# Optimization experiments

Measured on AMD Instinct MI355X. Metric: run time of the kernel, lower is better.

Reference implementation:

```python
import jax, jax.numpy as jnp
import numpy as np

B, S, D_MODEL, H, DK, DV, DOUT = 8, 2048, 1024, 1, 512, 512, 1024
EPS = 1e-6
TEMP = DK ** 0.5


def _ln(x, g, b):
    # LayerNorm over last dim, eps=1e-6, affine
    m = jnp.mean(x, axis=-1, keepdims=True)
    v = jnp.mean((x - m) ** 2, axis=-1, keepdims=True)
    return (x - m) * jax.lax.rsqrt(v + EPS) * g + b


def setup_inputs() -> dict:
    key = jax.random.key(0)
    ks = jax.random.split(key, 16)
    s = 0.02
    return {
        "q": jax.random.normal(ks[0], (B, S, D_MODEL), jnp.float32),
        "k": jax.random.normal(ks[1], (B, S, D_MODEL), jnp.float32),
        "v": jax.random.normal(ks[2], (B, S, D_MODEL), jnp.float32),
        "mask": jnp.ones((B, S, S), jnp.int32),
        "Wq": jax.random.normal(ks[3], (D_MODEL, H * DK), jnp.float32) * s,
        "bq": jnp.zeros((H * DK,), jnp.float32),
        "Wk": jax.random.normal(ks[4], (D_MODEL, H * DK), jnp.float32) * s,
        "bk": jnp.zeros((H * DK,), jnp.float32),
        "Wv": jax.random.normal(ks[5], (D_MODEL, H * DV), jnp.float32) * s,
        "bv": jnp.zeros((H * DV,), jnp.float32),
        "g_q": jnp.ones((H * DK,), jnp.float32),
        "be_q": jnp.zeros((H * DK,), jnp.float32),
        "g_k": jnp.ones((H * DK,), jnp.float32),
        "be_k": jnp.zeros((H * DK,), jnp.float32),
        "g_v": jnp.ones((H * DV,), jnp.float32),
        "be_v": jnp.zeros((H * DV,), jnp.float32),
        "W1": jax.random.normal(ks[6], (H * DV, H * DV), jnp.float32) * s,
        "b1": jnp.zeros((H * DV,), jnp.float32),
        "W2": jax.random.normal(ks[7], (H * DV, DOUT), jnp.float32) * s,
        "b2": jnp.zeros((DOUT,), jnp.float32),
    }


def reference(q, k, v, mask, Wq, bq, Wk, bk, Wv, bv, g_q, be_q, g_k, be_k, g_v, be_v, W1, b1, W2, b2):
    # QKV projections, viewed as (B, S, H, d)
    qp = (q @ Wq + bq).reshape(B, S, H, DK)
    kp = (k @ Wk + bk).reshape(B, S, H, DK)
    vp = (v @ Wv + bv).reshape(B, S, H, DV)
    residual = qp
    # per-(token,head) LayerNorm over last dim (valid only because H == 1 in source)
    qn = jnp.swapaxes(_ln(qp, g_q, be_q), 1, 2)  # (B, H, S, DK)
    kn = jnp.swapaxes(_ln(kp, g_k, be_k), 1, 2)
    vn = jnp.swapaxes(_ln(vp, g_v, be_v), 1, 2)
    # scaled dot-product attention with mask
    scores = jnp.einsum('bhqd,bhkd->bhqk', qn / TEMP, kn)
    scores = jnp.where(mask[:, None, :, :] == 0, -1e9, scores)
    attn = jax.nn.softmax(scores, axis=-1)
    out = jnp.einsum('bhqk,bhkd->bhqd', attn, vn)
    out = jnp.swapaxes(out, 1, 2).reshape(B, S, H * DV)
    # trailing 2-layer MLP
    out = jax.nn.relu(out @ W1 + b1) @ W2 + b2
    return (out, residual, jnp.squeeze(attn))
```

## Files before the change

### kernel.cpp

```cpp
#include <hip/hip_runtime.h>
#include <hip/hip_bf16.h>

typedef __attribute__((ext_vector_type(8))) short short8;
typedef __attribute__((ext_vector_type(4))) short short4v;
typedef __attribute__((ext_vector_type(4))) float f32x4;

#define INV_TEMP 0.044194173824159216f

__device__ __forceinline__ ushort f2bf(float f) {
  unsigned u = __float_as_uint(f);
  unsigned r = (u + 0x7FFFu + ((u >> 16) & 1u)) >> 16;
  return (ushort)r;
}
__device__ __forceinline__ float bf2f(ushort u) {
  union { unsigned i; float f; } x; x.i = ((unsigned)u) << 16; return x.f;
}

__device__ __forceinline__ void gload_lds16(const void* g, void* l) {
  __builtin_amdgcn_global_load_lds(
      (const __attribute__((address_space(1))) unsigned int*)(unsigned long long)(uintptr_t)g,
      (__attribute__((address_space(3))) unsigned int*)(unsigned)(uintptr_t)l,
      16, 0, 0);
}

__global__ __launch_bounds__(256)
void transpose_cvt_w(const float* __restrict__ W, ushort* __restrict__ WT, int K, int N) {
  __shared__ float tile[32][33];
  const int n0 = blockIdx.x * 32, k0 = blockIdx.y * 32;
  const int tx = threadIdx.x & 31, ty = threadIdx.x >> 5;
  #pragma unroll
  for (int i = ty; i < 32; i += 8)
    tile[i][tx] = W[(long)(k0 + i) * N + n0 + tx];
  __syncthreads();
  #pragma unroll
  for (int i = ty; i < 32; i += 8)
    WT[(long)(n0 + i) * K + k0 + tx] = f2bf(tile[tx][i]);
}

__global__ __launch_bounds__(256)
void transpose_cvt_w3(const float* __restrict__ W0, const float* __restrict__ W1,
                      const float* __restrict__ W2, ushort* __restrict__ T0,
                      ushort* __restrict__ T1, ushort* __restrict__ T2, int K, int N) {
  __shared__ float tile[32][33];
  const int z = blockIdx.z;
  const float* W = z == 0 ? W0 : (z == 1 ? W1 : W2);
  ushort* WT = z == 0 ? T0 : (z == 1 ? T1 : T2);
  const int n0 = blockIdx.x * 32, k0 = blockIdx.y * 32;
  const int tx = threadIdx.x & 31, ty = threadIdx.x >> 5;
  #pragma unroll
  for (int i = ty; i < 32; i += 8)
    tile[i][tx] = W[(long)(k0 + i) * N + n0 + tx];
  __syncthreads();
  #pragma unroll
  for (int i = ty; i < 32; i += 8)
    WT[(long)(n0 + i) * K + k0 + tx] = f2bf(tile[tx][i]);
}

__global__ __launch_bounds__(256)
void transpose_bf16(const ushort* __restrict__ in, ushort* __restrict__ out, int S, int D) {
  __shared__ ushort tile[32][33];
  const ushort* inb = in + (long)blockIdx.z * S * D;
  ushort* outb = out + (long)blockIdx.z * S * D;
  const int d0 = blockIdx.x * 32, s0 = blockIdx.y * 32;
  const int tx = threadIdx.x & 31, ty = threadIdx.x >> 5;
  #pragma unroll
  for (int i = ty; i < 32; i += 8)
    tile[i][tx] = inb[(long)(s0 + i) * D + d0 + tx];
  __syncthreads();
  #pragma unroll
  for (int i = ty; i < 32; i += 8)
    outb[(long)(d0 + i) * S + s0 + tx] = tile[tx][i];
}

__global__ __launch_bounds__(256)
void ln3_kernel(const float* __restrict__ Xq, const float* __restrict__ Xk,
                const float* __restrict__ Xv,
                const float* __restrict__ gq, const float* __restrict__ beq,
                const float* __restrict__ gk, const float* __restrict__ bek,
                const float* __restrict__ gv, const float* __restrict__ bev,
                ushort* __restrict__ Oq, ushort* __restrict__ Ok, ushort* __restrict__ Ov) {
  const int which = blockIdx.y;
  const float* X = which == 0 ? Xq : (which == 1 ? Xk : Xv);
  const float* g = which == 0 ? gq : (which == 1 ? gk : gv);
  const float* be = which == 0 ? beq : (which == 1 ? bek : bev);
  ushort* out = which == 0 ? Oq : (which == 1 ? Ok : Ov);
  const float scale = which == 0 ? INV_TEMP : 1.0f;

  const int row = blockIdx.x * 4 + (threadIdx.x >> 6);
  const int lane = threadIdx.x & 63;
  const float* x = X + (long)row * 512 + lane * 8;
  f32x4 v0 = *(const f32x4*)x;
  f32x4 v1 = *(const f32x4*)(x + 4);
  float s = v0[0]+v0[1]+v0[2]+v0[3]+v1[0]+v1[1]+v1[2]+v1[3];
  float ss = v0[0]*v0[0]+v0[1]*v0[1]+v0[2]*v0[2]+v0[3]*v0[3]
           + v1[0]*v1[0]+v1[1]*v1[1]+v1[2]*v1[2]+v1[3]*v1[3];
  #pragma unroll
  for (int off = 32; off; off >>= 1) { s += __shfl_xor(s, off); ss += __shfl_xor(ss, off); }
  const float mean = s * (1.0f/512.0f);
  const float var  = ss * (1.0f/512.0f) - mean*mean;
  const float rs = rsqrtf(var + 1e-6f);
  f32x4 g0 = *(const f32x4*)(g + lane*8);
  f32x4 g1 = *(const f32x4*)(g + lane*8 + 4);
  f32x4 b0 = *(const f32x4*)(be + lane*8);
  f32x4 b1 = *(const f32x4*)(be + lane*8 + 4);
  union { short8 v; ushort u[8]; } o;
  #pragma unroll
  for (int j = 0; j < 4; j++) o.u[j]     = f2bf(((v0[j]-mean)*rs*g0[j] + b0[j]) * scale);
  #pragma unroll
  for (int j = 0; j < 4; j++) o.u[4 + j] = f2bf(((v1[j]-mean)*rs*g1[j] + b1[j]) * scale);
  *(short8*)(out + (long)row * 512 + lane * 8) = o.v;
}

__global__ __launch_bounds__(256)
void softmax_finalize(const ushort* __restrict__ Pb, const float* __restrict__ partial,
                      float* __restrict__ attn_f32, float* __restrict__ invZ) {
  const long row = blockIdx.x;
  const long zb = row >> 11;
  const long s = row & 2047;
  const int t = threadIdx.x;
  float z = 0.f;
  #pragma unroll
  for (int j = 0; j < 16; j++) z += partial[((zb * 16 + j) << 11) + s];
  const float inv = 1.0f / z;
  if (t == 0) invZ[row] = inv;
  const ushort* pb = Pb + (row << 11);
  float* po = attn_f32 + (row << 11);
  short8 vv = *(const short8*)(pb + t * 8);
  f32x4 o0, o1;
  #pragma unroll
  for (int j = 0; j < 4; j++) o0[j] = bf2f((ushort)vv[j]) * inv;
  #pragma unroll
  for (int j = 0; j < 4; j++) o1[j] = bf2f((ushort)vv[4 + j]) * inv;
  *(f32x4*)(po + t * 8) = o0;
  *(f32x4*)(po + t * 8 + 4) = o1;
}

template<int EPI, bool HAS_BIAS, bool OUT_BF16, bool A_F32>
__global__ __launch_bounds__(256)
void gemm_tn(const void* __restrict__ Av, const ushort* __restrict__ Bt,
             const float* __restrict__ bias, const int* __restrict__ mask,
             float* __restrict__ Cf, ushort* __restrict__ Cb,
             float* __restrict__ partial, const float* __restrict__ invZ,
             int M, int N, int K,
             long sA, long sB, long sC, long sMask) {
  __shared__ ushort As[128 * 64];
  __shared__ ushort Bs[128 * 64];
  const int tid = threadIdx.x;
  const int lane = tid & 63;
  const int wave = tid >> 6;
  const int wr = wave >> 1, wc = wave & 1;

  const int gx = gridDim.x, gy = gridDim.y;
  int lin = blockIdx.x + gx * (blockIdx.y + gy * blockIdx.z);
  const int nwg = gx * gy * (int)gridDim.z;
  int swz = lin;
  if ((nwg & 7) == 0) {
    const int q8 = nwg >> 3;
    swz = (lin & 7) * q8 + (lin >> 3);
  }
  const int bx = swz % gx;
  const int tmp = swz / gx;
  const int by = tmp % gy;
  const int bz = tmp / gy;

  const long zb = bz;
  const ushort* Ab = (const ushort*)Av + zb * sA + (long)by * 128 * K;
  const float*  Af = (const float*)Av + zb * sA + (long)by * 128 * K;
  const ushort* Bb = Bt + zb * sB + (long)bx * 128 * K;

  f32x4 acc[4][4];
  #pragma unroll
  for (int m = 0; m < 4; m++)
    #pragma unroll
    for (int n = 0; n < 4; n++)
      acc[m][n] = f32x4{0.f, 0.f, 0.f, 0.f};

  for (int kt = 0; kt < K; kt += 64) {
    #pragma unroll
    for (int i = 0; i < 4; i++) {
      const int c = i * 256 + tid;
      const int row = c >> 3;
      const int g = c & 7;
      const int gsrc = g ^ (row & 7);
      gload_lds16(Bb + (long)row * K + kt + gsrc * 8, (char*)Bs + c * 16);
      if constexpr (A_F32) {
        const f32x4 u0 = *(const f32x4*)(Af + (long)row * K + kt + g * 8);
        const f32x4 u1 = *(const f32x4*)(Af + (long)row * K + kt + g * 8 + 4);
        union { short8 s; ushort u[8]; } o;
        #pragma unroll
        for (int j = 0; j < 4; j++) { o.u[j] = f2bf(u0[j]); o.u[4 + j] = f2bf(u1[j]); }
        *(short8*)((char*)As + ((row << 7) | ((g << 4) ^ ((row & 7) << 4)))) = o.s;
      } else {
        gload_lds16(Ab + (long)row * K + kt + gsrc * 8, (char*)As + c * 16);
      }
    }
    __syncthreads();
    #pragma unroll
    for (int ks = 0; ks < 2; ks++) {
      short8 af[4], bfr[4];
      const int kb = ks * 64 + ((lane >> 4) << 4);
      #pragma unroll
      for (int m = 0; m < 4; m++) {
        const int row = wr * 64 + m * 16 + (lane & 15);
        af[m] = *(const short8*)((const char*)As + ((row << 7) | (kb ^ ((row & 7) << 4))));
      }
      #pragma unroll
      for (int n = 0; n < 4; n++) {
        const int col = wc * 64 + n * 16 + (lane & 15);
        bfr[n] = *(const short8*)((const char*)Bs + ((col << 7) | (kb ^ ((col & 7) << 4))));
      }
      #pragma unroll
      for (int m = 0; m < 4; m++)
        #pragma unroll
        for (int n = 0; n < 4; n++)
          acc[m][n] = __builtin_amdgcn_mfma_f32_16x16x32_bf16(af[m], bfr[n], acc[m][n], 0, 0, 0);
    }
    __syncthreads();
  }

  const int colbase = bx * 128 + wc * 64;
  const int rowbase = by * 128 + wr * 64;
  const int c_lane = lane & 15;
  const int r_lane = (lane >> 4) << 2;

  float rs_acc[4][4];
  if constexpr (EPI == 2) {
    #pragma unroll
    for (int m = 0; m < 4; m++)
      #pragma unroll
      for (int r4 = 0; r4 < 4; r4++) rs_acc[m][r4] = 0.f;
  }

  #pragma unroll
  for (int n = 0; n < 4; n++) {
    const int col = colbase + n * 16 + c_lane;
    const float bv = HAS_BIAS ? bias[col] : 0.0f;
    #pragma unroll
    for (int m = 0; m < 4; m++) {
      const int rbase = rowbase + m * 16 + r_lane;
      #pragma unroll
      for (int r4 = 0; r4 < 4; r4++) {
        const int row = rbase + r4;
        float vv = acc[m][n][r4] + bv;
        if constexpr (EPI == 1) vv = fmaxf(vv, 0.0f);
        if constexpr (EPI == 2) {
          const int mk = mask[zb * sMask + (long)row * N + col];
          vv = mk ? __expf(vv) : 0.0f;
          rs_acc[m][r4] += vv;
        }
        if constexpr (EPI == 3) vv *= invZ[zb * 2048 + row];
        const long off = zb * sC + (long)row * N + col;
        if constexpr (OUT_BF16) Cb[off] = f2bf(vv);
        else                    Cf[off] = vv;
      }
    }
  }

  if constexpr (EPI == 2) {
    float (*red)[128] = (float(*)[128])As;
    #pragma unroll
    for (int m = 0; m < 4; m++)
      #pragma unroll
      for (int r4 = 0; r4 < 4; r4++) {
        float vsum = rs_acc[m][r4];
        vsum += __shfl_xor(vsum, 1);
        vsum += __shfl_xor(vsum, 2);
        vsum += __shfl_xor(vsum, 4);
        vsum += __shfl_xor(vsum, 8);
        if (c_lane == 0) red[wc][wr * 64 + m * 16 + r_lane + r4] = vsum;
      }
    __syncthreads();
    if (tid < 128)
      partial[((long)zb * 16 + bx) * 2048 + by * 128 + tid] = red[0][tid] + red[1][tid];
  }
}

extern "C" void kernel_launch(void* const* d_in, const int* in_sizes, int n_in,
                              void* d_out, int out_size, void* d_ws, size_t ws_size,
                              hipStream_t stream) {
  const float* q    = (const float*)d_in[0];
  const float* k    = (const float*)d_in[1];
  const float* v    = (const float*)d_in[2];
  const int*   mask = (const int*)d_in[3];
  const float* Wq   = (const float*)d_in[4];
  const float* bq   = (const float*)d_in[5];
  const float* Wk   = (const float*)d_in[6];
  const float* bk   = (const float*)d_in[7];
  const float* Wv   = (const float*)d_in[8];
  const float* bv   = (const float*)d_in[9];
  const float* g_q  = (const float*)d_in[10];
  const float* be_q = (const float*)d_in[11];
  const float* g_k  = (const float*)d_in[12];
  const float* be_k = (const float*)d_in[13];
  const float* g_v  = (const float*)d_in[14];
  const float* be_v = (const float*)d_in[15];
  const float* W1   = (const float*)d_in[16];
  const float* b1   = (const float*)d_in[17];
  const float* W2   = (const float*)d_in[18];
  const float* b2   = (const float*)d_in[19];

  float* out_mlp  = (float*)d_out;
  float* out_res  = out_mlp + 16777216L;
  float* out_attn = out_res + 8388608L;

  char* w = (char*)d_ws;
  ushort* qn      = (ushort*)(w);
  ushort* kn      = (ushort*)(w + 16777216UL);
  float*  kp      = (float*)(w + 33554432UL);
  ushort* attn_bf = (ushort*)(w + 33554432UL);
  float*  vp      = (float*)(w + 67108864UL);
  ushort* vn      = (ushort*)(w + 100663296UL);
  ushort* vnT     = (ushort*)(w + 117440512UL);
  ushort* pv      = (ushort*)(w + 134217728UL);
  ushort* h       = (ushort*)(w + 150994944UL);
  ushort* wqT     = (ushort*)(w + 167772160UL);
  ushort* wkT     = (ushort*)(w + 168820736UL);
  ushort* wvT     = (ushort*)(w + 169869312UL);
  ushort* w1T     = (ushort*)(w + 170917888UL);
  ushort* w2T     = (ushort*)(w + 171442176UL);
  float*  partial = (float*)(w + 172490752UL);
  float*  invZ    = (float*)(w + 173539328UL);

  dim3 blk(256);

  transpose_cvt_w3<<<dim3(16, 32, 3), blk, 0, stream>>>(Wq, Wk, Wv, wqT, wkT, wvT, 1024, 512);
  transpose_cvt_w<<<dim3(16, 16), blk, 0, stream>>>(W1, w1T, 512, 512);
  transpose_cvt_w<<<dim3(32, 16), blk, 0, stream>>>(W2, w2T, 512, 1024);

  gemm_tn<0, true, false, true><<<dim3(4, 128, 1), blk, 0, stream>>>(
      q, wqT, bq, nullptr, out_res, nullptr, nullptr, nullptr,
      16384, 512, 1024, 0, 0, 0, 0);
  gemm_tn<0, true, false, true><<<dim3(4, 128, 1), blk, 0, stream>>>(
      k, wkT, bk, nullptr, kp, nullptr, nullptr, nullptr,
      16384, 512, 1024, 0, 0, 0, 0);
  gemm_tn<0, true, false, true><<<dim3(4, 128, 1), blk, 0, stream>>>(
      v, wvT, bv, nullptr, vp, nullptr, nullptr, nullptr,
      16384, 512, 1024, 0, 0, 0, 0);

  ln3_kernel<<<dim3(4096, 3), blk, 0, stream>>>(
      out_res, kp, vp, g_q, be_q, g_k, be_k, g_v, be_v, qn, kn, vn);

  transpose_bf16<<<dim3(16, 64, 8), blk, 0, stream>>>(vn, vnT, 2048, 512);

  gemm_tn<2, false, true, false><<<dim3(16, 16, 8), blk, 0, stream>>>(
      qn, kn, nullptr, mask, nullptr, attn_bf, partial, nullptr,
      2048, 2048, 512,
      (long)2048 * 512, (long)2048 * 512, (long)2048 * 2048, (long)2048 * 2048);

  softmax_finalize<<<16384, blk, 0, stream>>>(attn_bf, partial, out_attn, invZ);

  gemm_tn<3, false, true, false><<<dim3(4, 16, 8), blk, 0, stream>>>(
      attn_bf, vnT, nullptr, nullptr, nullptr, pv, nullptr, invZ,
      2048, 512, 2048,
      (long)2048 * 2048, (long)512 * 2048, (long)2048 * 512, 0);

  gemm_tn<1, true, true, false><<<dim3(4, 128, 1), blk, 0, stream>>>(
      pv, w1T, b1, nullptr, nullptr, h, nullptr, nullptr,
      16384, 512, 512, 0, 0, 0, 0);
  gemm_tn<0, true, false, false><<<dim3(8, 128, 1), blk, 0, stream>>>(
      h, w2T, b2, nullptr, out_mlp, nullptr, nullptr, nullptr,
      16384, 1024, 512, 0, 0, 0, 0);
}
```

Before: 424.4 us.

## Fuse attention-probability write into PV GEMM and store K/V projections as bf16

The standalone softmax finalize pass is replaced by a small invZ reduction. The normalized fp32 attention matrix is now written from the PV GEMM's shared-memory A tiles by the bx==0 blocks, which saves a separate full read of the bf16 probabilities. K and V projections are stored as bf16 instead of fp32, halving their write and LayerNorm read traffic, at some cost in precision before normalization. The weight transpose kernels are merged into one launch.

```diff
diff --git a/kernel.cpp b/kernel.cpp
--- a/kernel.cpp
+++ b/kernel.cpp
@@ -24,27 +24,19 @@
 }
 
 __global__ __launch_bounds__(256)
-void transpose_cvt_w(const float* __restrict__ W, ushort* __restrict__ WT, int K, int N) {
+void transpose_cvt_all(const float* __restrict__ Wq, const float* __restrict__ Wk,
+                       const float* __restrict__ Wv, const float* __restrict__ W1,
+                       const float* __restrict__ W2,
+                       ushort* __restrict__ Tq, ushort* __restrict__ Tk,
+                       ushort* __restrict__ Tv, ushort* __restrict__ T1,
+                       ushort* __restrict__ T2) {
+  const int z = blockIdx.z;
+  const int K = (z < 3) ? 1024 : 512;
+  const int N = (z == 4) ? 1024 : 512;
+  if (blockIdx.x * 32 >= N || blockIdx.y * 32 >= K) return;
+  const float* W = z == 0 ? Wq : (z == 1 ? Wk : (z == 2 ? Wv : (z == 3 ? W1 : W2)));
+  ushort* WT = z == 0 ? Tq : (z == 1 ? Tk : (z == 2 ? Tv : (z == 3 ? T1 : T2)));
   __shared__ float tile[32][33];
-  const int n0 = blockIdx.x * 32, k0 = blockIdx.y * 32;
-  const int tx = threadIdx.x & 31, ty = threadIdx.x >> 5;
-  #pragma unroll
-  for (int i = ty; i < 32; i += 8)
-    tile[i][tx] = W[(long)(k0 + i) * N + n0 + tx];
-  __syncthreads();
-  #pragma unroll
-  for (int i = ty; i < 32; i += 8)
-    WT[(long)(n0 + i) * K + k0 + tx] = f2bf(tile[tx][i]);
-}
-
-__global__ __launch_bounds__(256)
-void transpose_cvt_w3(const float* __restrict__ W0, const float* __restrict__ W1,
-                      const float* __restrict__ W2, ushort* __restrict__ T0,
-                      ushort* __restrict__ T1, ushort* __restrict__ T2, int K, int N) {
-  __shared__ float tile[32][33];
-  const int z = blockIdx.z;
-  const float* W = z == 0 ? W0 : (z == 1 ? W1 : W2);
-  ushort* WT = z == 0 ? T0 : (z == 1 ? T1 : T2);
   const int n0 = blockIdx.x * 32, k0 = blockIdx.y * 32;
   const int tx = threadIdx.x & 31, ty = threadIdx.x >> 5;
   #pragma unroll
@@ -73,14 +65,13 @@
 }
 
 __global__ __launch_bounds__(256)
-void ln3_kernel(const float* __restrict__ Xq, const float* __restrict__ Xk,
-                const float* __restrict__ Xv,
+void ln3_kernel(const float* __restrict__ Xq, const ushort* __restrict__ Xk,
+                const ushort* __restrict__ Xv,
                 const float* __restrict__ gq, const float* __restrict__ beq,
                 const float* __restrict__ gk, const float* __restrict__ bek,
                 const float* __restrict__ gv, const float* __restrict__ bev,
                 ushort* __restrict__ Oq, ushort* __restrict__ Ok, ushort* __restrict__ Ov) {
   const int which = blockIdx.y;
-  const float* X = which == 0 ? Xq : (which == 1 ? Xk : Xv);
   const float* g = which == 0 ? gq : (which == 1 ? gk : gv);
   const float* be = which == 0 ? beq : (which == 1 ? bek : bev);
   ushort* out = which == 0 ? Oq : (which == 1 ? Ok : Ov);
@@ -88,9 +79,17 @@
 
   const int row = blockIdx.x * 4 + (threadIdx.x >> 6);
   const int lane = threadIdx.x & 63;
-  const float* x = X + (long)row * 512 + lane * 8;
-  f32x4 v0 = *(const f32x4*)x;
-  f32x4 v1 = *(const f32x4*)(x + 4);
+  f32x4 v0, v1;
+  if (which == 0) {
+    const float* x = Xq + (long)row * 512 + lane * 8;
+    v0 = *(const f32x4*)x;
+    v1 = *(const f32x4*)(x + 4);
+  } else {
+    const ushort* x = (which == 1 ? Xk : Xv) + (long)row * 512 + lane * 8;
+    short8 vv = *(const short8*)x;
+    #pragma unroll
+    for (int j = 0; j < 4; j++) { v0[j] = bf2f((ushort)vv[j]); v1[j] = bf2f((ushort)vv[4 + j]); }
+  }
   float s = v0[0]+v0[1]+v0[2]+v0[3]+v1[0]+v1[1]+v1[2]+v1[3];
   float ss = v0[0]*v0[0]+v0[1]*v0[1]+v0[2]*v0[2]+v0[3]*v0[3]
            + v1[0]*v1[0]+v1[1]*v1[1]+v1[2]*v1[2]+v1[3]*v1[3];
@@ -112,27 +111,13 @@
 }
 
 __global__ __launch_bounds__(256)
-void softmax_finalize(const ushort* __restrict__ Pb, const float* __restrict__ partial,
-                      float* __restrict__ attn_f32, float* __restrict__ invZ) {
-  const long row = blockIdx.x;
-  const long zb = row >> 11;
-  const long s = row & 2047;
-  const int t = threadIdx.x;
+void invz_reduce(const float* __restrict__ partial, float* __restrict__ invZ) {
+  const int r = blockIdx.x * 256 + threadIdx.x;
+  const int zb = r >> 11, s = r & 2047;
   float z = 0.f;
   #pragma unroll
   for (int j = 0; j < 16; j++) z += partial[((zb * 16 + j) << 11) + s];
-  const float inv = 1.0f / z;
-  if (t == 0) invZ[row] = inv;
-  const ushort* pb = Pb + (row << 11);
-  float* po = attn_f32 + (row << 11);
-  short8 vv = *(const short8*)(pb + t * 8);
-  f32x4 o0, o1;
-  #pragma unroll
-  for (int j = 0; j < 4; j++) o0[j] = bf2f((ushort)vv[j]) * inv;
-  #pragma unroll
-  for (int j = 0; j < 4; j++) o1[j] = bf2f((ushort)vv[4 + j]) * inv;
-  *(f32x4*)(po + t * 8) = o0;
-  *(f32x4*)(po + t * 8 + 4) = o1;
+  invZ[r] = 1.0f / z;
 }
 
 template<int EPI, bool HAS_BIAS, bool OUT_BF16, bool A_F32>
@@ -145,6 +130,7 @@
              long sA, long sB, long sC, long sMask) {
   __shared__ ushort As[128 * 64];
   __shared__ ushort Bs[128 * 64];
+  __shared__ float zloc[128];
   const int tid = threadIdx.x;
   const int lane = tid & 63;
   const int wave = tid >> 6;
@@ -167,6 +153,11 @@
   const ushort* Ab = (const ushort*)Av + zb * sA + (long)by * 128 * K;
   const float*  Af = (const float*)Av + zb * sA + (long)by * 128 * K;
   const ushort* Bb = Bt + zb * sB + (long)bx * 128 * K;
+  const int rowbase0 = by * 128;
+
+  if constexpr (EPI == 3) {
+    if (tid < 128) zloc[tid] = invZ[zb * 2048 + rowbase0 + tid];
+  }
 
   f32x4 acc[4][4];
   #pragma unroll
@@ -195,6 +186,29 @@
       }
     }
     __syncthreads();
+
+    if constexpr (EPI == 3) {
+      if (bx == 0) {
+        #pragma unroll
+        for (int i = 0; i < 4; i++) {
+          const int c = i * 256 + tid;
+          const int row = c >> 3;
+          const int j = c & 7;
+          short8 p8 = *(const short8*)((const char*)As + ((row << 7) | ((j ^ (row & 7)) << 4)));
+          const float iz = zloc[row];
+          f32x4 o0, o1;
+          #pragma unroll
+          for (int jj = 0; jj < 4; jj++) {
+            o0[jj] = bf2f((ushort)p8[jj]) * iz;
+            o1[jj] = bf2f((ushort)p8[4 + jj]) * iz;
+          }
+          float* dst = Cf + zb * 4194304L + (long)(rowbase0 + row) * 2048 + kt + j * 8;
+          *(f32x4*)dst = o0;
+          *(f32x4*)(dst + 4) = o1;
+        }
+      }
+    }
+
     #pragma unroll
     for (int ks = 0; ks < 2; ks++) {
       short8 af[4], bfr[4];
@@ -248,7 +262,7 @@
           vv = mk ? __expf(vv) : 0.0f;
           rs_acc[m][r4] += vv;
         }
-        if constexpr (EPI == 3) vv *= invZ[zb * 2048 + row];
+        if constexpr (EPI == 3) vv *= zloc[wr * 64 + m * 16 + r_lane + r4];
         const long off = zb * sC + (long)row * N + col;
         if constexpr (OUT_BF16) Cb[off] = f2bf(vv);
         else                    Cf[off] = vv;
@@ -306,9 +320,9 @@
   char* w = (char*)d_ws;
   ushort* qn      = (ushort*)(w);
   ushort* kn      = (ushort*)(w + 16777216UL);
-  float*  kp      = (float*)(w + 33554432UL);
+  ushort* kp_bf   = (ushort*)(w + 33554432UL);
+  ushort* vp_bf   = (ushort*)(w + 50331648UL);
   ushort* attn_bf = (ushort*)(w + 33554432UL);
-  float*  vp      = (float*)(w + 67108864UL);
   ushort* vn      = (ushort*)(w + 100663296UL);
   ushort* vnT     = (ushort*)(w + 117440512UL);
   ushort* pv      = (ushort*)(w + 134217728UL);
@@ -323,22 +337,21 @@
 
   dim3 blk(256);
 
-  transpose_cvt_w3<<<dim3(16, 32, 3), blk, 0, stream>>>(Wq, Wk, Wv, wqT, wkT, wvT, 1024, 512);
-  transpose_cvt_w<<<dim3(16, 16), blk, 0, stream>>>(W1, w1T, 512, 512);
-  transpose_cvt_w<<<dim3(32, 16), blk, 0, stream>>>(W2, w2T, 512, 1024);
+  transpose_cvt_all<<<dim3(32, 32, 5), blk, 0, stream>>>(
+      Wq, Wk, Wv, W1, W2, wqT, wkT, wvT, w1T, w2T);
 
   gemm_tn<0, true, false, true><<<dim3(4, 128, 1), blk, 0, stream>>>(
       q, wqT, bq, nullptr, out_res, nullptr, nullptr, nullptr,
       16384, 512, 1024, 0, 0, 0, 0);
-  gemm_tn<0, true, false, true><<<dim3(4, 128, 1), blk, 0, stream>>>(
-      k, wkT, bk, nullptr, kp, nullptr, nullptr, nullptr,
+  gemm_tn<0, true, true, true><<<dim3(4, 128, 1), blk, 0, stream>>>(
+      k, wkT, bk, nullptr, nullptr, kp_bf, nullptr, nullptr,
       16384, 512, 1024, 0, 0, 0, 0);
-  gemm_tn<0, true, false, true><<<dim3(4, 128, 1), blk, 0, stream>>>(
-      v, wvT, bv, nullptr, vp, nullptr, nullptr, nullptr,
+  gemm_tn<0, true, true, true><<<dim3(4, 128, 1), blk, 0, stream>>>(
+      v, wvT, bv, nullptr, nullptr, vp_bf, nullptr, nullptr,
       16384, 512, 1024, 0, 0, 0, 0);
 
   ln3_kernel<<<dim3(4096, 3), blk, 0, stream>>>(
-      out_res, kp, vp, g_q, be_q, g_k, be_k, g_v, be_v, qn, kn, vn);
+      out_res, kp_bf, vp_bf, g_q, be_q, g_k, be_k, g_v, be_v, qn, kn, vn);
 
   transpose_bf16<<<dim3(16, 64, 8), blk, 0, stream>>>(vn, vnT, 2048, 512);
 
@@ -347,10 +360,10 @@
       2048, 2048, 512,
       (long)2048 * 512, (long)2048 * 512, (long)2048 * 2048, (long)2048 * 2048);
 
-  softmax_finalize<<<16384, blk, 0, stream>>>(attn_bf, partial, out_attn, invZ);
+  invz_reduce<<<64, blk, 0, stream>>>(partial, invZ);
 
   gemm_tn<3, false, true, false><<<dim3(4, 16, 8), blk, 0, stream>>>(
-      attn_bf, vnT, nullptr, nullptr, nullptr, pv, nullptr, invZ,
+      attn_bf, vnT, nullptr, nullptr, out_attn, pv, nullptr, invZ,
       2048, 512, 2048,
       (long)2048 * 2048, (long)512 * 2048, (long)2048 * 512, 0);
 
```

Measured after the change: 421.8 us. Within noise of the previous version (-0.6%).
